# Performance work log

Measured on AMD Instinct MI355X. Metric: run time of the kernel, lower is better.

The kernel has to match this reference:

```python
import jax, jax.numpy as jnp
import numpy as np

TEMPERATURE = 0.1
EPS = 1e-8  # torch cosine_similarity eps
NEG_FILL = -9e15

def setup_inputs() -> dict:
    key = jax.random.key(0)
    stacked_batch = jax.random.normal(key, (8192, 128), dtype=jnp.float32)
    return {"stacked_batch": stacked_batch}

def reference(stacked_batch) -> jnp.ndarray:
    n = stacked_batch.shape[0]
    # cosine similarity = normalized GEMM (equivalent to torch broadcast form)
    norm = jnp.maximum(jnp.linalg.norm(stacked_batch, axis=-1, keepdims=True), EPS)
    z = stacked_batch / norm                      # [N, D]
    sim = jnp.matmul(z, z.T) / TEMPERATURE        # [N, N]
    # mask self-similarity on the diagonal
    idx = jnp.arange(n)
    sim = sim.at[idx, idx].set(NEG_FILL)
    # positive pair for row i is column (i + N/2) mod N
    pos_cols = (idx + n // 2) % n
    pos = sim[idx, pos_cols]                      # [N]
    loss = jax.scipy.special.logsumexp(sim, axis=-1) - pos
    return loss.mean()
```

## Files before the change

### kernel.cpp

```cpp
#include <hip/hip_runtime.h>
#include <hip/hip_bf16.h>

#define N 8192
#define D 128
#define HALF_N 4096
#define SQRT_SCALE_LOG2E 3.79828236f
#define LN2 0.693147180559945f

#define BLOCK_ROWS 256
#define COLS_PER_ITER 64
#define COL_SPLITS 16
#define COLS_PER_BLOCK (N / COL_SPLITS)
#define ITERS (COLS_PER_BLOCK / COLS_PER_ITER)

typedef short frag8 __attribute__((ext_vector_type(8)));
typedef float f32x4 __attribute__((ext_vector_type(4)));
typedef const __attribute__((address_space(1))) unsigned int* gbl_u32p;
typedef __attribute__((address_space(3))) unsigned int* lds_u32p;

#define OFF_POS    0
#define OFF_PSUMS  (N)
#define OFF_ACC    (N + COL_SPLITS * N)
#define OFF_Z_BYTES ((OFF_ACC + 64) * 4)

__device__ __forceinline__ unsigned short f2bf(float f) {
    unsigned int u = __float_as_uint(f);
    u += 0x7FFFu + ((u >> 16) & 1u);
    return (unsigned short)(u >> 16);
}

__global__ __launch_bounds__(256) void k_normalize(const float* __restrict__ x,
                                                   unsigned short* __restrict__ z,
                                                   float* __restrict__ acc0) {
    const int row  = blockIdx.x * 4 + (threadIdx.x >> 6);
    const int lane = threadIdx.x & 63;
    float2 v = ((const float2*)x)[row * 64 + lane];
    float s = v.x * v.x + v.y * v.y;
    #pragma unroll
    for (int m = 32; m >= 1; m >>= 1) s += __shfl_xor(s, m);
    float inv = SQRT_SCALE_LOG2E / fmaxf(sqrtf(s), 1e-8f);
    ushort2 o;
    o.x = f2bf(v.x * inv);
    o.y = f2bf(v.y * inv);
    ((ushort2*)z)[row * 64 + lane] = o;
    if (blockIdx.x == 0 && threadIdx.x == 0) acc0[0] = 0.0f;
}

__device__ __forceinline__ void stage_tile(const unsigned short* __restrict__ z,
                                           unsigned short* ldsbuf,
                                           int colbase, int wave,
                                           const int* stg_src) {
    const unsigned short* zc = z + (size_t)colbase * D;
    #pragma unroll
    for (int u = 0; u < 4; ++u) {
        __builtin_amdgcn_global_load_lds((gbl_u32p)(zc + stg_src[u]),
                                         (lds_u32p)(ldsbuf + (wave * 16 + u * 4) * D),
                                         16, 0, 0);
    }
}

__global__ __launch_bounds__(256, 2) void k_simloss(const unsigned short* __restrict__ z,
                                                    float* __restrict__ psums,
                                                    float* __restrict__ pos) {
    __shared__ unsigned short lds[2][COLS_PER_ITER * D];

    const int tid  = threadIdx.x;
    const int wave = tid >> 6;
    const int lane = tid & 63;
    const int l15  = lane & 15;
    const int quad = lane >> 4;
    const int l7   = l15 & 7;
    const int wrow = blockIdx.x * BLOCK_ROWS + wave * 64;
    const int colbase0 = blockIdx.y * COLS_PER_BLOCK;
    const int posbase  = (wrow + HALF_N) & (N - 1);

    int stg_src[4];
    #pragma unroll
    for (int u = 0; u < 4; ++u) {
        int r = wave * 16 + u * 4 + (lane >> 4);
        stg_src[u] = r * D + ((l15 ^ (r & 7)) << 3);
    }

    int boff[4];
    #pragma unroll
    for (int q = 0; q < 4; ++q)
        boff[q] = l15 * D + (((quad + 4 * q) ^ l7) << 3);

    frag8 a[4][4];
    #pragma unroll
    for (int s = 0; s < 4; ++s) {
        const uint4* p = (const uint4*)&z[(wrow + s * 16 + l15) * D + quad * 8];
        #pragma unroll
        for (int q = 0; q < 4; ++q) {
            uint4 t = p[q * 4];
            a[s][q] = *(frag8*)&t;
        }
    }

    float sums[4][4];
    #pragma unroll
    for (int s = 0; s < 4; ++s)
        #pragma unroll
        for (int r = 0; r < 4; ++r) sums[s][r] = 0.0f;

    stage_tile(z, &lds[0][0], colbase0, wave, stg_src);
    __syncthreads();

    for (int it = 0; it < ITERS; ++it) {
        if (it + 1 < ITERS)
            stage_tile(z, &lds[(it + 1) & 1][0], colbase0 + (it + 1) * COLS_PER_ITER, wave, stg_src);

        const int colbase = colbase0 + it * COLS_PER_ITER;
        const bool isDiag = (colbase == wrow);
        const bool isPos  = (colbase == posbase);
        const unsigned short* lb = &lds[it & 1][0];

        #pragma unroll
        for (int c = 0; c < 4; ++c) {
            f32x4 acc[4];
            #pragma unroll
            for (int s = 0; s < 4; ++s) acc[s] = (f32x4){0.f, 0.f, 0.f, 0.f};
            #pragma unroll
            for (int q = 0; q < 4; ++q) {
                frag8 b = *(const frag8*)&lb[c * (16 * D) + boff[q]];
                #pragma unroll
                for (int s = 0; s < 4; ++s)
                    acc[s] = __builtin_amdgcn_mfma_f32_16x16x32_bf16(a[s][q], b, acc[s], 0, 0, 0);
            }
            if (isDiag | isPos) {
                #pragma unroll
                for (int s = 0; s < 4; ++s)
                    #pragma unroll
                    for (int r = 0; r < 4; ++r) {
                        float v = acc[s][r];
                        float e = __builtin_amdgcn_exp2f(v);
                        if (c == s) {
                            bool hit = (l15 == quad * 4 + r);
                            if (isDiag && hit) e = 0.0f;
                            if (isPos  && hit) pos[wrow + s * 16 + quad * 4 + r] = v * LN2;
                        }
                        sums[s][r] += e;
                    }
            } else {
                #pragma unroll
                for (int s = 0; s < 4; ++s)
                    #pragma unroll
                    for (int r = 0; r < 4; ++r)
                        sums[s][r] += __builtin_amdgcn_exp2f(acc[s][r]);
            }
        }
        __syncthreads();
    }

    #pragma unroll
    for (int s = 0; s < 4; ++s)
        #pragma unroll
        for (int r = 0; r < 4; ++r) {
            float v = sums[s][r];
            v += __shfl_xor(v, 1);
            v += __shfl_xor(v, 2);
            v += __shfl_xor(v, 4);
            v += __shfl_xor(v, 8);
            if (l15 == 0)
                psums[blockIdx.y * N + wrow + s * 16 + quad * 4 + r] = v;
        }
}

__global__ __launch_bounds__(1024) void k_rowloss(const float* __restrict__ psums,
                                                  const float* __restrict__ pos,
                                                  float* __restrict__ acc0) {
    const int row = blockIdx.x * 1024 + threadIdx.x;
    float t = 0.0f;
    #pragma unroll
    for (int s = 0; s < COL_SPLITS; ++s) t += psums[s * N + row];
    float loss = __logf(t) - pos[row];
    #pragma unroll
    for (int m = 32; m >= 1; m >>= 1) loss += __shfl_xor(loss, m);
    __shared__ float p[16];
    if ((threadIdx.x & 63) == 0) p[threadIdx.x >> 6] = loss;
    __syncthreads();
    if (threadIdx.x == 0) {
        float s = 0.0f;
        #pragma unroll
        for (int w = 0; w < 16; ++w) s += p[w];
        atomicAdd(acc0, s);
    }
}

__global__ void k_final(const float* __restrict__ acc0, float* __restrict__ out) {
    out[0] = acc0[0] * (1.0f / N);
}

extern "C" void kernel_launch(void* const* d_in, const int* in_sizes, int n_in,
                              void* d_out, int out_size, void* d_ws, size_t ws_size,
                              hipStream_t stream) {
    const float* x = (const float*)d_in[0];
    float* wsf   = (float*)d_ws;
    float* pos   = wsf + OFF_POS;
    float* psums = wsf + OFF_PSUMS;
    float* acc0  = wsf + OFF_ACC;
    unsigned short* z = (unsigned short*)((char*)d_ws + OFF_Z_BYTES);

    k_normalize<<<N / 4, 256, 0, stream>>>(x, z, acc0);
    dim3 g2(N / BLOCK_ROWS, COL_SPLITS);
    k_simloss<<<g2, 256, 0, stream>>>(z, psums, pos);
    k_rowloss<<<N / 1024, 1024, 0, stream>>>(psums, pos, acc0);
    k_final<<<1, 1, 0, stream>>>(acc0, (float*)d_out);
}
```

Measured before the change: 82.02 us.

## Switch to 32x32x16 MFMA with 4-buffer LDS pipeline and single barrier

Replaces the 16x16x32 MFMA tiling with 32x32x16 bf16 MFMAs, two 32-row A tiles per wave, and reworked B fragment addressing and output row mapping. LDS staging moves from double buffering to four buffers with prefetch distance two. The two __syncthreads per iteration are replaced by explicit vmcnt waits plus one s_barrier. The aim is fewer LDS B reads per FLOP and better overlap of global-to-LDS loads with compute. The cost is more accumulator and A-fragment registers and fragile hand-written wait counts.

Result: slower. 87.57 us (+6.8%).

```diff
diff --git a/kernel.cpp b/kernel.cpp
--- a/kernel.cpp
+++ b/kernel.cpp
@@ -12,9 +12,10 @@
 #define COL_SPLITS 16
 #define COLS_PER_BLOCK (N / COL_SPLITS)
 #define ITERS (COLS_PER_BLOCK / COLS_PER_ITER)
+#define NBUF 4
 
 typedef short frag8 __attribute__((ext_vector_type(8)));
-typedef float f32x4 __attribute__((ext_vector_type(4)));
+typedef float f32x16 __attribute__((ext_vector_type(16)));
 typedef const __attribute__((address_space(1))) unsigned int* gbl_u32p;
 typedef __attribute__((address_space(3))) unsigned int* lds_u32p;
 
@@ -62,14 +63,13 @@
 __global__ __launch_bounds__(256, 2) void k_simloss(const unsigned short* __restrict__ z,
                                                     float* __restrict__ psums,
                                                     float* __restrict__ pos) {
-    __shared__ unsigned short lds[2][COLS_PER_ITER * D];
+    __shared__ unsigned short lds[NBUF][COLS_PER_ITER * D];
 
     const int tid  = threadIdx.x;
     const int wave = tid >> 6;
     const int lane = tid & 63;
-    const int l15  = lane & 15;
-    const int quad = lane >> 4;
-    const int l7   = l15 & 7;
+    const int c31  = lane & 31;
+    const int hi   = lane >> 5;
     const int wrow = blockIdx.x * BLOCK_ROWS + wave * 64;
     const int colbase0 = blockIdx.y * COLS_PER_BLOCK;
     const int posbase  = (wrow + HALF_N) & (N - 1);
@@ -78,91 +78,107 @@
     #pragma unroll
     for (int u = 0; u < 4; ++u) {
         int r = wave * 16 + u * 4 + (lane >> 4);
-        stg_src[u] = r * D + ((l15 ^ (r & 7)) << 3);
-    }
-
-    int boff[4];
-    #pragma unroll
-    for (int q = 0; q < 4; ++q)
-        boff[q] = l15 * D + (((quad + 4 * q) ^ l7) << 3);
-
-    frag8 a[4][4];
-    #pragma unroll
-    for (int s = 0; s < 4; ++s) {
-        const uint4* p = (const uint4*)&z[(wrow + s * 16 + l15) * D + quad * 8];
-        #pragma unroll
-        for (int q = 0; q < 4; ++q) {
-            uint4 t = p[q * 4];
-            a[s][q] = *(frag8*)&t;
+        stg_src[u] = r * D + (((lane & 15) ^ (r & 7)) << 3);
+    }
+
+    frag8 a[2][8];
+    #pragma unroll
+    for (int s = 0; s < 2; ++s) {
+        const unsigned short* ap = &z[(wrow + s * 32 + c31) * D + hi * 8];
+        #pragma unroll
+        for (int kc = 0; kc < 8; ++kc)
+            a[s][kc] = *(const frag8*)(ap + kc * 16);
+    }
+    asm volatile("" ::: "memory");
+
+    float sums[2][16];
+    #pragma unroll
+    for (int s = 0; s < 2; ++s)
+        #pragma unroll
+        for (int r = 0; r < 16; ++r) sums[s][r] = 0.0f;
+
+    stage_tile(z, &lds[0][0], colbase0 + 0 * COLS_PER_ITER, wave, stg_src);
+    stage_tile(z, &lds[1][0], colbase0 + 1 * COLS_PER_ITER, wave, stg_src);
+
+    #pragma unroll 1
+    for (int t = 0; t < ITERS; ++t) {
+        if (t + 2 < ITERS) {
+            stage_tile(z, &lds[(t + 2) & 3][0], colbase0 + (t + 2) * COLS_PER_ITER, wave, stg_src);
+            asm volatile("s_waitcnt vmcnt(8)" ::: "memory");
+        } else if (t + 2 == ITERS) {
+            asm volatile("s_waitcnt vmcnt(4)" ::: "memory");
+        } else {
+            asm volatile("s_waitcnt vmcnt(0)" ::: "memory");
         }
-    }
-
-    float sums[4][4];
-    #pragma unroll
-    for (int s = 0; s < 4; ++s)
-        #pragma unroll
-        for (int r = 0; r < 4; ++r) sums[s][r] = 0.0f;
-
-    stage_tile(z, &lds[0][0], colbase0, wave, stg_src);
-    __syncthreads();
-
-    for (int it = 0; it < ITERS; ++it) {
-        if (it + 1 < ITERS)
-            stage_tile(z, &lds[(it + 1) & 1][0], colbase0 + (it + 1) * COLS_PER_ITER, wave, stg_src);
-
-        const int colbase = colbase0 + it * COLS_PER_ITER;
-        const bool isDiag = (colbase == wrow);
-        const bool isPos  = (colbase == posbase);
-        const unsigned short* lb = &lds[it & 1][0];
-
-        #pragma unroll
-        for (int c = 0; c < 4; ++c) {
-            f32x4 acc[4];
+        __builtin_amdgcn_s_barrier();
+        asm volatile("" ::: "memory");
+
+        const unsigned short* lb = &lds[t & 3][0];
+        const int colbase = colbase0 + t * COLS_PER_ITER;
+
+        #pragma unroll
+        for (int ct = 0; ct < 2; ++ct) {
+            const int col0 = colbase + ct * 32;
+            f32x16 acc0, acc1;
             #pragma unroll
-            for (int s = 0; s < 4; ++s) acc[s] = (f32x4){0.f, 0.f, 0.f, 0.f};
+            for (int i = 0; i < 16; ++i) { acc0[i] = 0.0f; acc1[i] = 0.0f; }
+
             #pragma unroll
-            for (int q = 0; q < 4; ++q) {
-                frag8 b = *(const frag8*)&lb[c * (16 * D) + boff[q]];
+            for (int kc = 0; kc < 8; ++kc) {
+                frag8 b = *(const frag8*)&lb[(ct * 32 + c31) * D +
+                                             (((kc * 2 + hi) ^ (c31 & 7)) << 3)];
+                acc0 = __builtin_amdgcn_mfma_f32_32x32x16_bf16(a[0][kc], b, acc0, 0, 0, 0);
+                acc1 = __builtin_amdgcn_mfma_f32_32x32x16_bf16(a[1][kc], b, acc1, 0, 0, 0);
+            }
+
+            const bool d0 = (col0 == wrow);
+            const bool d1 = (col0 == wrow + 32);
+            const bool p0 = (col0 == posbase);
+            const bool p1 = (col0 == posbase + 32);
+            if (d0 | d1 | p0 | p1) {
                 #pragma unroll
-                for (int s = 0; s < 4; ++s)
-                    acc[s] = __builtin_amdgcn_mfma_f32_16x16x32_bf16(a[s][q], b, acc[s], 0, 0, 0);
-            }
-            if (isDiag | isPos) {
-                #pragma unroll
-                for (int s = 0; s < 4; ++s)
-                    #pragma unroll
-                    for (int r = 0; r < 4; ++r) {
-                        float v = acc[s][r];
+                for (int r = 0; r < 16; ++r) {
+                    const int rowoff = (r & 3) + 8 * (r >> 2) + 4 * hi;
+                    const bool hit = (c31 == rowoff);
+                    {
+                        float v = acc0[r];
                         float e = __builtin_amdgcn_exp2f(v);
-                        if (c == s) {
-                            bool hit = (l15 == quad * 4 + r);
-                            if (isDiag && hit) e = 0.0f;
-                            if (isPos  && hit) pos[wrow + s * 16 + quad * 4 + r] = v * LN2;
-                        }
-                        sums[s][r] += e;
+                        if (d0 && hit) e = 0.0f;
+                        if (p0 && hit) pos[wrow + rowoff] = v * LN2;
+                        sums[0][r] += e;
                     }
+                    {
+                        float v = acc1[r];
+                        float e = __builtin_amdgcn_exp2f(v);
+                        if (d1 && hit) e = 0.0f;
+                        if (p1 && hit) pos[wrow + 32 + rowoff] = v * LN2;
+                        sums[1][r] += e;
+                    }
+                }
             } else {
                 #pragma unroll
-                for (int s = 0; s < 4; ++s)
-                    #pragma unroll
-                    for (int r = 0; r < 4; ++r)
-                        sums[s][r] += __builtin_amdgcn_exp2f(acc[s][r]);
+                for (int r = 0; r < 16; ++r) {
+                    sums[0][r] += __builtin_amdgcn_exp2f(acc0[r]);
+                    sums[1][r] += __builtin_amdgcn_exp2f(acc1[r]);
+                }
             }
         }
-        __syncthreads();
-    }
-
-    #pragma unroll
-    for (int s = 0; s < 4; ++s)
-        #pragma unroll
-        for (int r = 0; r < 4; ++r) {
+    }
+
+    #pragma unroll
+    for (int s = 0; s < 2; ++s)
+        #pragma unroll
+        for (int r = 0; r < 16; ++r) {
             float v = sums[s][r];
             v += __shfl_xor(v, 1);
             v += __shfl_xor(v, 2);
             v += __shfl_xor(v, 4);
             v += __shfl_xor(v, 8);
-            if (l15 == 0)
-                psums[blockIdx.y * N + wrow + s * 16 + quad * 4 + r] = v;
+            v += __shfl_xor(v, 16);
+            if (c31 == 0) {
+                const int row = wrow + s * 32 + (r & 3) + 8 * (r >> 2) + 4 * hi;
+                psums[blockIdx.y * N + row] = v;
+            }
         }
 }
 
```
